# Performance work log

Hardware: AMD Instinct MI355X
Metric: run time of the kernel (lower is better)

The kernel has to match this reference:

```python
import jax, jax.numpy as jnp
import numpy as np

DIM = 1024
NUM_HEADS = 16
HEAD_DIM = DIM // NUM_HEADS
SCALE = HEAD_DIM ** -0.5


def setup_inputs() -> dict:
    key = jax.random.key(0)
    k1, k2, k3, k4, k5 = jax.random.split(key, 5)
    B, N, C = 2, 2048, DIM
    x = jax.random.normal(k1, (B, N, C), dtype=jnp.float32)
    # nn.Linear(dim, 3*dim, bias=False): weight shape [3*dim, dim]
    w_qkv = jax.random.normal(k2, (3 * C, C), dtype=jnp.float32) * (C ** -0.5)
    # nn.Linear(dim, dim): weight [dim, dim], bias [dim]
    w_proj = jax.random.normal(k3, (C, C), dtype=jnp.float32) * (C ** -0.5)
    b_proj = jax.random.normal(k4, (C,), dtype=jnp.float32) * 0.02
    return {"x": x, "w_qkv": w_qkv, "w_proj": w_proj, "b_proj": b_proj}


def reference(x, w_qkv, w_proj, b_proj):
    B, N, C = x.shape
    H, D = NUM_HEADS, HEAD_DIM
    # qkv: [B, N, 3C] -> [3, B, H, N, D]
    qkv = (x @ w_qkv.T).reshape(B, N, 3, H, D).transpose(2, 0, 3, 1, 4)
    q, k, v = qkv[0], qkv[1], qkv[2]
    # attention scores [B, H, N, N]
    attn = jnp.einsum("bhnd,bhmd->bhnm", q, k) * SCALE
    attn = jax.nn.softmax(attn, axis=-1)
    # dropout p=0.0 -> identity (eval mode)
    out = jnp.einsum("bhnm,bhmd->bhnd", attn, v)  # [B, H, N, D]
    out = out.transpose(0, 2, 1, 3).reshape(B, N, C)
    return out @ w_proj.T + b_proj
```

## Files before the change

### kernel.cpp

```cpp
#include <hip/hip_runtime.h>
#include <hip/hip_bf16.h>
#include <cstdint>

#define DEV __device__ __forceinline__

typedef float f32x4 __attribute__((ext_vector_type(4)));
typedef short bf16x8 __attribute__((ext_vector_type(8)));
typedef unsigned short u16;
typedef unsigned int u32;

constexpr int Bb = 2, Nn = 2048, Cc = 1024, Hh = 16, Dd = 64;
constexpr float QSCALE = 0.18033688011112042f;

DEV u16 f2b(float f) {
  unsigned u = __float_as_uint(f);
  u += 0x7FFFu + ((u >> 16) & 1u);
  return (u16)(u >> 16);
}

DEV void gload_lds16(const u16* g, u16* l) {
  __builtin_amdgcn_global_load_lds(
      (const __attribute__((address_space(1))) void*)g,
      (__attribute__((address_space(3))) void*)l, 16, 0, 0);
}

DEV int swz(int row, int byteInRow) {
  return row * 128 + (byteInRow ^ ((row & 7) << 4));
}
DEV int swzp(int row, int byteInRow) {
  return row * 64 + (byteInRow ^ ((((row >> 2) + row) & 3) << 4));
}

DEV u32 cvtpk(float lo, float hi) {
  u32 r;
  asm("v_cvt_pk_bf16_f32 %0, %1, %2" : "=v"(r) : "v"(lo), "v"(hi));
  return r;
}
DEV void pl32swap(u32& a, u32& b) {
  asm("v_permlane32_swap_b32 %0, %1" : "+v"(a), "+v"(b));
}
DEV void pl16swap(u32& a, u32& b) {
  asm("v_permlane16_swap_b32 %0, %1" : "+v"(a), "+v"(b));
}

#if __has_builtin(__builtin_amdgcn_exp2f)
DEV float fast_exp2(float x) { return __builtin_amdgcn_exp2f(x); }
#else
DEV float fast_exp2(float x) { return exp2f(x); }
#endif

__global__ void cvt_all(const float* __restrict__ x, u16* __restrict__ xb,
                        const float* __restrict__ wq, u16* __restrict__ wqb,
                        const float* __restrict__ wp, u16* __restrict__ wpb) {
  constexpr int n1 = 4096 * 1024 / 4, n2 = 3072 * 1024 / 4, n3 = 1024 * 1024 / 4;
  constexpr int nQ = 1024 * 1024 / 4;
  int idx = blockIdx.x * blockDim.x + threadIdx.x;
  int stride = gridDim.x * blockDim.x;
  for (int i = idx; i < n1 + n2 + n3; i += stride) {
    const float* in; u16* out; int j;
    float sc = 1.f;
    if (i < n1) { in = x; out = xb; j = i; }
    else if (i < n1 + n2) { in = wq; out = wqb; j = i - n1; if (j < nQ) sc = QSCALE; }
    else { in = wp; out = wpb; j = i - n1 - n2; }
    float4 v = ((const float4*)in)[j];
    ushort4 o;
    o.x = f2b(v.x * sc); o.y = f2b(v.y * sc); o.z = f2b(v.z * sc); o.w = f2b(v.w * sc);
    ((ushort4*)out)[j] = o;
  }
}

__global__ __launch_bounds__(256) void gemm_qkv(
    const u16* __restrict__ A, const u16* __restrict__ W, u16* __restrict__ qkv_out) {
  constexpr int K = 1024, NT = K / 32;
  __shared__ __align__(16) u16 As[3][128 * 32];
  __shared__ __align__(16) u16 Bs[3][128 * 32];
  const int t = threadIdx.x, lane = t & 63;
  const int wm = t >> 7, wn = (t >> 6) & 1;
  const int bid = blockIdx.x;
  const int wg = (bid & 7) * 96 + (bid >> 3);
  const int bx = wg % 24, by = wg / 24;
  const int m0 = by * 128, n0 = bx * 128;
  const int fr = lane & 15, g = lane >> 4;

  const int srow = t >> 2;
  const int scp = (t & 3) ^ (((t >> 2) + (t >> 4)) & 3);
  const u16* gA = A + (size_t)(m0 + srow) * K + scp * 8;
  const u16* gW = W + (size_t)(n0 + srow) * K + scp * 8;

  f32x4 acc[4][4] = {};

#define STAGEQ(tile, buf)                                              \
  {                                                                    \
    const int k0_ = (tile) * 32;                                       \
    gload_lds16(gA + k0_, &As[buf][t * 8]);                            \
    gload_lds16(gA + k0_ + (size_t)64 * K, &As[buf][t * 8 + 2048]);    \
    gload_lds16(gW + k0_, &Bs[buf][t * 8]);                            \
    gload_lds16(gW + k0_ + (size_t)64 * K, &Bs[buf][t * 8 + 2048]);    \
  }

  STAGEQ(0, 0);
  STAGEQ(1, 1);
  asm volatile("s_waitcnt vmcnt(4)" ::: "memory");
  __builtin_amdgcn_s_barrier();

  for (int tt = 0; tt < NT; ++tt) {
    const int cur = tt % 3;
    const int nxt2 = (tt + 2 < NT) ? tt + 2 : NT - 1;
    STAGEQ(nxt2, (tt + 2) % 3);
    const char* Ac = (const char*)As[cur];
    const char* Bc = (const char*)Bs[cur];
    bf16x8 af[4], bfr[4];
#pragma unroll
    for (int i = 0; i < 4; ++i)
      af[i] = *(const bf16x8*)(Ac + swzp(wm * 64 + i * 16 + fr, g * 16));
#pragma unroll
    for (int j = 0; j < 4; ++j)
      bfr[j] = *(const bf16x8*)(Bc + swzp(wn * 64 + j * 16 + fr, g * 16));
    __builtin_amdgcn_s_setprio(1);
#pragma unroll
    for (int i = 0; i < 4; ++i)
#pragma unroll
      for (int j = 0; j < 4; ++j)
        acc[i][j] = __builtin_amdgcn_mfma_f32_16x16x32_bf16(af[i], bfr[j], acc[i][j], 0, 0, 0);
    __builtin_amdgcn_s_setprio(0);
    asm volatile("s_waitcnt vmcnt(4)" ::: "memory");
    __builtin_amdgcn_s_barrier();
  }

  const int rg = g * 4;
#pragma unroll
  for (int mi = 0; mi < 4; ++mi) {
#pragma unroll
    for (int ni = 0; ni < 4; ++ni) {
      const int col = n0 + wn * 64 + ni * 16 + fr;
      const int s = col >> 10, h = (col >> 6) & 15, d = col & 63;
      const int row0 = m0 + wm * 64 + mi * 16 + rg;
      const int b = row0 >> 11, nb = row0 & 2047;
      if (s == 2) {
        ushort4 o4;
        o4.x = f2b(acc[mi][ni][0]); o4.y = f2b(acc[mi][ni][1]);
        o4.z = f2b(acc[mi][ni][2]); o4.w = f2b(acc[mi][ni][3]);
        const size_t off = (size_t)2 * Bb * Hh * Nn * Dd +
                           (((size_t)b * Hh + h) * Dd + d) * Nn + nb;
        *(ushort4*)&qkv_out[off] = o4;
      } else {
#pragma unroll
        for (int r = 0; r < 4; ++r) {
          const size_t off = ((((size_t)s * Bb + b) * Hh + h) * Nn + (nb + r)) * Dd + d;
          qkv_out[off] = f2b(acc[mi][ni][r]);
        }
      }
    }
  }
#undef STAGEQ
}

__global__ __launch_bounds__(256, 2) void gemm_proj(
    const u16* __restrict__ A, const u16* __restrict__ W,
    float* __restrict__ fout, const float* __restrict__ bias) {
  constexpr int K = 1024, Nmat = 1024, NT = K / 32;
  __shared__ __align__(16) u16 As[2][64 * 32];
  __shared__ __align__(16) u16 Bs[2][128 * 32];
  const int t = threadIdx.x, lane = t & 63, w = t >> 6;
  const int bid = blockIdx.x;
  const int wg = (bid & 7) * 64 + (bid >> 3);
  const int bx = wg & 7, by = wg >> 3;
  const int m0 = by * 64, n0 = bx * 128;
  const int fr = lane & 15, g = lane >> 4;

  const int srow = t >> 2;
  const int scp = (t & 3) ^ (((t >> 2) + (t >> 4)) & 3);
  const u16* gA = A + (size_t)(m0 + srow) * K + scp * 8;
  const u16* gW = W + (size_t)(n0 + srow) * K + scp * 8;

  f32x4 acc[4][2] = {};

#define STAGEP(tile, buf)                                              \
  {                                                                    \
    const int k0_ = (tile) * 32;                                       \
    gload_lds16(gA + k0_, &As[buf][t * 8]);                            \
    gload_lds16(gW + k0_, &Bs[buf][t * 8]);                            \
    gload_lds16(gW + k0_ + (size_t)64 * K, &Bs[buf][t * 8 + 2048]);    \
  }

  STAGEP(0, 0);
  __syncthreads();

  for (int tt = 0; tt < NT; ++tt) {
    const int cur = tt & 1;
    if (tt + 1 < NT) STAGEP(tt + 1, cur ^ 1);
    const char* Ac = (const char*)As[cur];
    const char* Bc = (const char*)Bs[cur];
    bf16x8 af[4], bfr[2];
#pragma unroll
    for (int i = 0; i < 4; ++i)
      af[i] = *(const bf16x8*)(Ac + swzp(i * 16 + fr, g * 16));
#pragma unroll
    for (int j = 0; j < 2; ++j)
      bfr[j] = *(const bf16x8*)(Bc + swzp(w * 32 + j * 16 + fr, g * 16));
    __builtin_amdgcn_s_setprio(1);
#pragma unroll
    for (int i = 0; i < 4; ++i)
#pragma unroll
      for (int j = 0; j < 2; ++j)
        acc[i][j] = __builtin_amdgcn_mfma_f32_16x16x32_bf16(af[i], bfr[j], acc[i][j], 0, 0, 0);
    __builtin_amdgcn_s_setprio(0);
    __syncthreads();
  }

  const int rg = g * 4;
#pragma unroll
  for (int i = 0; i < 4; ++i)
#pragma unroll
    for (int j = 0; j < 2; ++j) {
      const int col = n0 + w * 32 + j * 16 + fr;
#pragma unroll
      for (int r = 0; r < 4; ++r) {
        const int row = m0 + i * 16 + rg + r;
        fout[(size_t)row * Nmat + col] = acc[i][j][r] + bias[col];
      }
    }
#undef STAGEP
}

__global__ __launch_bounds__(512, 4) void attn_fwd(
    const u16* __restrict__ Qg, const u16* __restrict__ Kg,
    const u16* __restrict__ Vtg, u16* __restrict__ Og) {
  __shared__ __align__(16) char smem[34816];
  const int t = threadIdx.x, lane = t & 63, w = t >> 6;
  const int qg = w >> 1, kh = w & 1;
  const int wg = ((blockIdx.x & 7) << 6) | (blockIdx.x >> 3);
  const int bh = wg >> 4;
  const int q0 = (wg & 15) * 128;
  const size_t base = (size_t)bh * Nn * Dd;
  const u16* Qb = Qg + base;
  const u16* Kb = Kg + base;
  const u16* Vb = Vtg + base;
  const int fr = lane & 15, g = lane >> 4;

  bf16x8 onesv;
  {
    union { u32 u[4]; bf16x8 v; } o_;
#pragma unroll
    for (int i = 0; i < 4; ++i) o_.u[i] = 0x3F803F80u;
    onesv = o_.v;
  }

  bf16x8 qf[2][2];
#pragma unroll
  for (int qt = 0; qt < 2; ++qt)
#pragma unroll
    for (int dc = 0; dc < 2; ++dc)
      qf[qt][dc] = *(const bf16x8*)&Qb[(size_t)(q0 + qg * 32 + qt * 16 + fr) * 64 + dc * 32 + g * 8];

  f32x4 ot[4][2] = {};
  float lse[2] = {0.f, 0.f};

  const int srow = t >> 3, scb = t & 7;
  const u16* kp = Kb + srow * 64 + scb * 8;
  const u16* vp = Vb + (size_t)srow * Nn + scb * 8;
  uint4 kreg, vreg;

#define LOADT(tile)                                        \
  {                                                        \
    kreg = *(const uint4*)(kp + (size_t)(tile) * 4096);    \
    vreg = *(const uint4*)(vp + (size_t)(tile) * 64);      \
  }
#define STORET(buf)                                        \
  {                                                        \
    char* kb_ = smem + (buf) * 16384;                      \
    *(uint4*)(kb_ + swz(srow, scb * 16)) = kreg;           \
    *(uint4*)(kb_ + 8192 + swz(srow, scb * 16)) = vreg;    \
  }

  LOADT(0);
  STORET(0);
  __syncthreads();

  for (int it = 0; it < 32; ++it) {
    const int cur = it & 1;
    const char* Kst = smem + cur * 16384;
    const char* Vst = Kst + 8192;
    if (it < 31) LOADT(it + 1);

    bf16x8 kf[2][2];
#pragma unroll
    for (int kvt = 0; kvt < 2; ++kvt)
#pragma unroll
      for (int dc = 0; dc < 2; ++dc)
        kf[kvt][dc] = *(const bf16x8*)(Kst + swz(kh * 32 + kvt * 16 + fr, dc * 64 + g * 16));
    f32x4 st[2][2] = {};
    __builtin_amdgcn_s_setprio(1);
#pragma unroll
    for (int dc = 0; dc < 2; ++dc)
#pragma unroll
      for (int kvt = 0; kvt < 2; ++kvt)
#pragma unroll
        for (int qt = 0; qt < 2; ++qt)
          st[kvt][qt] = __builtin_amdgcn_mfma_f32_16x16x32_bf16(kf[kvt][dc], qf[qt][dc], st[kvt][qt], 0, 0, 0);
    __builtin_amdgcn_s_setprio(0);

#pragma unroll
    for (int kvt = 0; kvt < 2; ++kvt)
#pragma unroll
      for (int qt = 0; qt < 2; ++qt)
#pragma unroll
        for (int r = 0; r < 4; ++r)
          st[kvt][qt][r] = fast_exp2(st[kvt][qt][r]);

    u32 pw[2][4];
#pragma unroll
    for (int qt = 0; qt < 2; ++qt) {
      u32 a0 = cvtpk(st[0][qt][0], st[0][qt][1]);
      u32 a1 = cvtpk(st[0][qt][2], st[0][qt][3]);
      u32 b0 = cvtpk(st[1][qt][0], st[1][qt][1]);
      u32 b1 = cvtpk(st[1][qt][2], st[1][qt][3]);
      pl32swap(a0, b0); pl16swap(a0, b0);
      pl32swap(a1, b1); pl16swap(a1, b1);
      pw[qt][0] = a0; pw[qt][1] = a1; pw[qt][2] = b0; pw[qt][3] = b1;
    }

    bf16x8 vf[4];
#pragma unroll
    for (int dt = 0; dt < 4; ++dt)
      vf[dt] = *(const bf16x8*)(Vst + swz(dt * 16 + fr, kh * 64 + g * 16));
    __builtin_amdgcn_s_setprio(1);
#pragma unroll
    for (int qt = 0; qt < 2; ++qt) {
      union { u32 u[4]; bf16x8 v; } pu;
      pu.u[0] = pw[qt][0]; pu.u[1] = pw[qt][1]; pu.u[2] = pw[qt][2]; pu.u[3] = pw[qt][3];
      f32x4 z = {0.f, 0.f, 0.f, 0.f};
      f32x4 rsv = __builtin_amdgcn_mfma_f32_16x16x32_bf16(onesv, pu.v, z, 0, 0, 0);
      lse[qt] += rsv[0];
#pragma unroll
      for (int dt = 0; dt < 4; ++dt)
        ot[dt][qt] = __builtin_amdgcn_mfma_f32_16x16x32_bf16(vf[dt], pu.v, ot[dt][qt], 0, 0, 0);
    }
    __builtin_amdgcn_s_setprio(0);

    if (it < 31) {
      STORET(cur ^ 1);
      __syncthreads();
    }
  }

  __syncthreads();
  float* Ob = (float*)(smem + qg * 8448);
  float* Lb = (float*)(smem + 33792 + qg * 128);
  if (kh) {
#pragma unroll
    for (int qt = 0; qt < 2; ++qt) {
#pragma unroll
      for (int dt = 0; dt < 4; ++dt)
#pragma unroll
        for (int r = 0; r < 4; ++r)
          Ob[(qt * 16 + fr) * 66 + dt * 16 + 4 * g + r] = ot[dt][qt][r];
      if (g == 0) Lb[qt * 16 + fr] = lse[qt];
    }
  }
  __syncthreads();
  if (!kh) {
    const int b = bh >> 4, h = bh & 15;
#pragma unroll
    for (int qt = 0; qt < 2; ++qt) {
      const float inv = 1.f / (lse[qt] + Lb[qt * 16 + fr]);
      const int tok = q0 + qg * 32 + qt * 16 + fr;
      const size_t rowbase = ((size_t)b * Nn + tok) * Cc + h * 64;
#pragma unroll
      for (int dt = 0; dt < 4; ++dt) {
        ushort4 o4;
        o4.x = f2b((ot[dt][qt][0] + Ob[(qt * 16 + fr) * 66 + dt * 16 + 4 * g + 0]) * inv);
        o4.y = f2b((ot[dt][qt][1] + Ob[(qt * 16 + fr) * 66 + dt * 16 + 4 * g + 1]) * inv);
        o4.z = f2b((ot[dt][qt][2] + Ob[(qt * 16 + fr) * 66 + dt * 16 + 4 * g + 2]) * inv);
        o4.w = f2b((ot[dt][qt][3] + Ob[(qt * 16 + fr) * 66 + dt * 16 + 4 * g + 3]) * inv);
        *(ushort4*)&Og[rowbase + dt * 16 + g * 4] = o4;
      }
    }
  }
#undef LOADT
#undef STORET
}

extern "C" void kernel_launch(void* const* d_in, const int* in_sizes, int n_in,
                              void* d_out, int out_size, void* d_ws, size_t ws_size,
                              hipStream_t stream) {
  const float* x      = (const float*)d_in[0];
  const float* w_qkv  = (const float*)d_in[1];
  const float* w_proj = (const float*)d_in[2];
  const float* b_proj = (const float*)d_in[3];
  float* out = (float*)d_out;

  u16* xb     = (u16*)d_ws;
  u16* wqkvb  = xb + (size_t)4096 * 1024;
  u16* wprojb = wqkvb + (size_t)3072 * 1024;
  u16* qkv    = wprojb + (size_t)1024 * 1024;
  u16* ows    = qkv + (size_t)3 * Bb * Hh * Nn * Dd;
  u16* q  = qkv;
  u16* k  = qkv + (size_t)Bb * Hh * Nn * Dd;
  u16* vt = k + (size_t)Bb * Hh * Nn * Dd;

  cvt_all<<<2048, 256, 0, stream>>>(x, xb, w_qkv, wqkvb, w_proj, wprojb);
  gemm_qkv<<<768, 256, 0, stream>>>(xb, wqkvb, qkv);
  attn_fwd<<<512, 512, 0, stream>>>(q, k, vt, ows);
  gemm_proj<<<512, 256, 0, stream>>>(ows, wprojb, out, b_proj);
}
```

Baseline: 107.7 us.

## Software-pipeline attention loop: overlap QK of next tile with softmax/PV of previous

Restructures the attention main loop into a two-stage software pipeline. The QK^T MFMAs for tile i are issued alongside the exp/convert and PV MFMAs for tile i-1. This needs a triple-buffered LDS ring (48KB instead of 34KB) and two score register sets, so matrix-core work can overlap the transcendental/pack work. In exchange it uses more registers and LDS, which at launch_bounds(512,4) may cut occupancy or cause spills.

```diff
diff --git a/kernel.cpp b/kernel.cpp
--- a/kernel.cpp
+++ b/kernel.cpp
@@ -226,7 +226,7 @@
 __global__ __launch_bounds__(512, 4) void attn_fwd(
     const u16* __restrict__ Qg, const u16* __restrict__ Kg,
     const u16* __restrict__ Vtg, u16* __restrict__ Og) {
-  __shared__ __align__(16) char smem[34816];
+  __shared__ __align__(16) char smem[49152];
   const int t = threadIdx.x, lane = t & 63, w = t >> 6;
   const int qg = w >> 1, kh = w & 1;
   const int wg = ((blockIdx.x & 7) << 6) | (blockIdx.x >> 3);
@@ -266,83 +266,87 @@
     kreg = *(const uint4*)(kp + (size_t)(tile) * 4096);    \
     vreg = *(const uint4*)(vp + (size_t)(tile) * 64);      \
   }
-#define STORET(buf)                                        \
+#define STORETP(bp)                                        \
   {                                                        \
-    char* kb_ = smem + (buf) * 16384;                      \
-    *(uint4*)(kb_ + swz(srow, scb * 16)) = kreg;           \
-    *(uint4*)(kb_ + 8192 + swz(srow, scb * 16)) = vreg;    \
-  }
+    *(uint4*)((bp) + swz(srow, scb * 16)) = kreg;          \
+    *(uint4*)((bp) + 8192 + swz(srow, scb * 16)) = vreg;   \
+  }
+#define QKSTEP(bp, SN)                                                          \
+  {                                                                             \
+    bf16x8 kf_[2][2];                                                           \
+    _Pragma("unroll") for (int kvt = 0; kvt < 2; ++kvt)                         \
+        _Pragma("unroll") for (int dc = 0; dc < 2; ++dc)                        \
+            kf_[kvt][dc] = *(const bf16x8*)((bp) +                              \
+                swz(kh * 32 + kvt * 16 + fr, dc * 64 + g * 16));                \
+    SN[0][0] = SN[0][1] = SN[1][0] = SN[1][1] = (f32x4){0.f, 0.f, 0.f, 0.f};    \
+    __builtin_amdgcn_s_setprio(1);                                              \
+    _Pragma("unroll") for (int dc = 0; dc < 2; ++dc)                            \
+        _Pragma("unroll") for (int kvt = 0; kvt < 2; ++kvt)                     \
+            _Pragma("unroll") for (int qt = 0; qt < 2; ++qt)                    \
+                SN[kvt][qt] = __builtin_amdgcn_mfma_f32_16x16x32_bf16(          \
+                    kf_[kvt][dc], qf[qt][dc], SN[kvt][qt], 0, 0, 0);            \
+    __builtin_amdgcn_s_setprio(0);                                              \
+  }
+#define FINSTEP(SO, vbp)                                                        \
+  {                                                                             \
+    _Pragma("unroll") for (int kvt = 0; kvt < 2; ++kvt)                         \
+        _Pragma("unroll") for (int qt = 0; qt < 2; ++qt)                        \
+            _Pragma("unroll") for (int r = 0; r < 4; ++r)                       \
+                SO[kvt][qt][r] = fast_exp2(SO[kvt][qt][r]);                     \
+    bf16x8 vf_[4];                                                              \
+    _Pragma("unroll") for (int dt = 0; dt < 4; ++dt)                            \
+        vf_[dt] = *(const bf16x8*)((vbp) + 8192 +                               \
+            swz(dt * 16 + fr, kh * 64 + g * 16));                               \
+    _Pragma("unroll") for (int qt = 0; qt < 2; ++qt) {                          \
+      u32 a0 = cvtpk(SO[0][qt][0], SO[0][qt][1]);                               \
+      u32 a1 = cvtpk(SO[0][qt][2], SO[0][qt][3]);                               \
+      u32 b0 = cvtpk(SO[1][qt][0], SO[1][qt][1]);                               \
+      u32 b1 = cvtpk(SO[1][qt][2], SO[1][qt][3]);                               \
+      pl32swap(a0, b0); pl16swap(a0, b0);                                       \
+      pl32swap(a1, b1); pl16swap(a1, b1);                                       \
+      union { u32 u[4]; bf16x8 v; } pu;                                         \
+      pu.u[0] = a0; pu.u[1] = a1; pu.u[2] = b0; pu.u[3] = b1;                   \
+      f32x4 z = {0.f, 0.f, 0.f, 0.f};                                           \
+      __builtin_amdgcn_s_setprio(1);                                            \
+      f32x4 rsv = __builtin_amdgcn_mfma_f32_16x16x32_bf16(onesv, pu.v, z, 0, 0, 0); \
+      lse[qt] += rsv[0];                                                        \
+      _Pragma("unroll") for (int dt = 0; dt < 4; ++dt)                          \
+          ot[dt][qt] = __builtin_amdgcn_mfma_f32_16x16x32_bf16(                 \
+              vf_[dt], pu.v, ot[dt][qt], 0, 0, 0);                              \
+      __builtin_amdgcn_s_setprio(0);                                            \
+    }                                                                           \
+  }
+#define ITER(i, SO, SN)                                    \
+  {                                                        \
+    if ((i) < 31) LOADT((i) + 1);                          \
+    QKSTEP(cur, SN);                                       \
+    FINSTEP(SO, prv);                                      \
+    if ((i) < 31) STORETP(nxt);                            \
+    __syncthreads();                                       \
+    char* tmp_ = prv; prv = cur; cur = nxt; nxt = tmp_;    \
+  }
+
+  char* prv = smem;
+  char* cur = smem + 16384;
+  char* nxt = smem + 32768;
+
+  f32x4 stA[2][2], stB[2][2];
 
   LOADT(0);
-  STORET(0);
+  STORETP(prv);
   __syncthreads();
-
-  for (int it = 0; it < 32; ++it) {
-    const int cur = it & 1;
-    const char* Kst = smem + cur * 16384;
-    const char* Vst = Kst + 8192;
-    if (it < 31) LOADT(it + 1);
-
-    bf16x8 kf[2][2];
-#pragma unroll
-    for (int kvt = 0; kvt < 2; ++kvt)
-#pragma unroll
-      for (int dc = 0; dc < 2; ++dc)
-        kf[kvt][dc] = *(const bf16x8*)(Kst + swz(kh * 32 + kvt * 16 + fr, dc * 64 + g * 16));
-    f32x4 st[2][2] = {};
-    __builtin_amdgcn_s_setprio(1);
-#pragma unroll
-    for (int dc = 0; dc < 2; ++dc)
-#pragma unroll
-      for (int kvt = 0; kvt < 2; ++kvt)
-#pragma unroll
-        for (int qt = 0; qt < 2; ++qt)
-          st[kvt][qt] = __builtin_amdgcn_mfma_f32_16x16x32_bf16(kf[kvt][dc], qf[qt][dc], st[kvt][qt], 0, 0, 0);
-    __builtin_amdgcn_s_setprio(0);
-
-#pragma unroll
-    for (int kvt = 0; kvt < 2; ++kvt)
-#pragma unroll
-      for (int qt = 0; qt < 2; ++qt)
-#pragma unroll
-        for (int r = 0; r < 4; ++r)
-          st[kvt][qt][r] = fast_exp2(st[kvt][qt][r]);
-
-    u32 pw[2][4];
-#pragma unroll
-    for (int qt = 0; qt < 2; ++qt) {
-      u32 a0 = cvtpk(st[0][qt][0], st[0][qt][1]);
-      u32 a1 = cvtpk(st[0][qt][2], st[0][qt][3]);
-      u32 b0 = cvtpk(st[1][qt][0], st[1][qt][1]);
-      u32 b1 = cvtpk(st[1][qt][2], st[1][qt][3]);
-      pl32swap(a0, b0); pl16swap(a0, b0);
-      pl32swap(a1, b1); pl16swap(a1, b1);
-      pw[qt][0] = a0; pw[qt][1] = a1; pw[qt][2] = b0; pw[qt][3] = b1;
-    }
-
-    bf16x8 vf[4];
-#pragma unroll
-    for (int dt = 0; dt < 4; ++dt)
-      vf[dt] = *(const bf16x8*)(Vst + swz(dt * 16 + fr, kh * 64 + g * 16));
-    __builtin_amdgcn_s_setprio(1);
-#pragma unroll
-    for (int qt = 0; qt < 2; ++qt) {
-      union { u32 u[4]; bf16x8 v; } pu;
-      pu.u[0] = pw[qt][0]; pu.u[1] = pw[qt][1]; pu.u[2] = pw[qt][2]; pu.u[3] = pw[qt][3];
-      f32x4 z = {0.f, 0.f, 0.f, 0.f};
-      f32x4 rsv = __builtin_amdgcn_mfma_f32_16x16x32_bf16(onesv, pu.v, z, 0, 0, 0);
-      lse[qt] += rsv[0];
-#pragma unroll
-      for (int dt = 0; dt < 4; ++dt)
-        ot[dt][qt] = __builtin_amdgcn_mfma_f32_16x16x32_bf16(vf[dt], pu.v, ot[dt][qt], 0, 0, 0);
-    }
-    __builtin_amdgcn_s_setprio(0);
-
-    if (it < 31) {
-      STORET(cur ^ 1);
-      __syncthreads();
-    }
-  }
+  LOADT(1);
+  QKSTEP(prv, stA);
+  STORETP(cur);
+  __syncthreads();
+
+  ITER(1, stA, stB);
+  for (int ii = 2; ii <= 30; ii += 2) {
+    ITER(ii, stB, stA);
+    ITER(ii + 1, stA, stB);
+  }
+
+  FINSTEP(stB, prv);
 
   __syncthreads();
   float* Ob = (float*)(smem + qg * 8448);
@@ -378,7 +382,10 @@
     }
   }
 #undef LOADT
-#undef STORET
+#undef STORETP
+#undef QKSTEP
+#undef FINSTEP
+#undef ITER
 }
 
 extern "C" void kernel_launch(void* const* d_in, const int* in_sizes, int n_in,
```

After: 110.3 us. 2.5% more time.
